# Optimization experiments

Measured on AMD Instinct MI355X. Metric: run time of the kernel, lower is better.

The kernel has to match this reference:

```python
import jax, jax.numpy as jnp
import numpy as np

N_NODES = 80000
N_EDGES = 160000
HID = 300
NODE_DIM = 133
EDGE_DIM = 14
N_GRAPHS = 1600


def setup_inputs() -> dict:
    key = jax.random.key(0)
    ks = jax.random.split(key, 32)
    s = 0.05
    half = N_EDGES // 2
    inp = {
        "x": jax.random.normal(ks[0], (N_NODES, NODE_DIM), jnp.float32),
        "edge_attr": jax.random.normal(ks[1], (N_EDGES, EDGE_DIM), jnp.float32),
        "W_atoms": jax.random.uniform(ks[2], (N_NODES,), jnp.float32),
        "eps": jax.random.normal(ks[3], (N_GRAPHS, HID), jnp.float32),
        "src_half": jax.random.randint(ks[4], (half,), 0, N_NODES, jnp.int32),
        "dst_half": jax.random.randint(ks[5], (half,), 0, N_NODES, jnp.int32),
        "batch": jnp.sort(jax.random.randint(ks[6], (N_NODES,), 0, N_GRAPHS, jnp.int32)),
    }
    def W(k, i, o):
        return jax.random.normal(k, (i, o), jnp.float32) * s
    def B(k, o):
        return jax.random.normal(k, (o,), jnp.float32) * s
    # tconv1 (first_linear=True): lin1 in=node+edge, atom_updater in=node+hid (with ReLU)
    inp["t_lin_w"] = W(ks[7], NODE_DIM + EDGE_DIM, HID); inp["t_lin_b"] = B(ks[8], HID)
    inp["t_mp_w"] = jax.random.normal(ks[9], (3, HID, HID), jnp.float32) * s
    inp["t_mp_b"] = jax.random.normal(ks[10], (3, HID), jnp.float32) * s
    inp["t_au_w"] = W(ks[11], NODE_DIM + HID, HID); inp["t_au_b"] = B(ks[12], HID)
    # mu conv (first_linear=False): lin2 in=hid+edge, atom_updater2 in=2*hid (no ReLU)
    inp["mu_lin_w"] = W(ks[13], HID + EDGE_DIM, HID); inp["mu_lin_b"] = B(ks[14], HID)
    inp["mu_mp_w"] = jax.random.normal(ks[15], (3, HID, HID), jnp.float32) * s
    inp["mu_mp_b"] = jax.random.normal(ks[16], (3, HID), jnp.float32) * s
    inp["mu_au_w"] = W(ks[17], 2 * HID, HID); inp["mu_au_b"] = B(ks[18], HID)
    # logvar conv (first_linear=False)
    inp["lv_lin_w"] = W(ks[19], HID + EDGE_DIM, HID); inp["lv_lin_b"] = B(ks[20], HID)
    inp["lv_mp_w"] = jax.random.normal(ks[21], (3, HID, HID), jnp.float32) * s
    inp["lv_mp_b"] = jax.random.normal(ks[22], (3, HID), jnp.float32) * s
    inp["lv_au_w"] = W(ks[23], 2 * HID, HID); inp["lv_au_b"] = B(ks[24], HID)
    return inp


def reference(x, edge_attr, W_atoms, eps, src_half, dst_half, batch,
              t_lin_w, t_lin_b, t_mp_w, t_mp_b, t_au_w, t_au_b,
              mu_lin_w, mu_lin_b, mu_mp_w, mu_mp_b, mu_au_w, mu_au_b,
              lv_lin_w, lv_lin_b, lv_mp_w, lv_mp_b, lv_au_w, lv_au_b):
    E = edge_attr.shape[0]
    half = E // 2
    N = x.shape[0]
    # directed edges come in reverse pairs: edge e and edge rev(e)
    src = jnp.concatenate([src_half, dst_half])
    dst = jnp.concatenate([dst_half, src_half])
    rev = jnp.concatenate([jnp.arange(half, E), jnp.arange(0, half)])
    relu = jax.nn.relu

    def mp_agg(h):
        # dest_is_origin sparse mm: for edge e=(u->v), sum h over edges k with
        # dst(k)==u, excluding the reverse edge (v->u)
        inc = jax.ops.segment_sum(h, dst, num_segments=N)  # [N, H]
        return inc[src] - h[rev]

    def conv(node_in, lin_w, lin_b, mp_w, mp_b, au_w, au_b, out_relu):
        h = relu(jnp.concatenate([node_in[src], edge_attr], axis=1) @ lin_w + lin_b)
        for i in range(3):  # three vec_scratch_MP_layers: relu(h + Lin(D @ h))
            h = relu(h + mp_agg(h) @ mp_w[i] + mp_b[i])
        # inc_edges_to_atom sparse mm: sum incident edge states per atom
        sum_inc = jax.ops.segment_sum(h, dst, num_segments=N)
        a = jnp.concatenate([node_in, sum_inc], axis=1) @ au_w + au_b
        return relu(a) if out_relu else a

    shared = conv(x, t_lin_w, t_lin_b, t_mp_w, t_mp_b, t_au_w, t_au_b, True)
    mu = conv(shared, mu_lin_w, mu_lin_b, mu_mp_w, mu_mp_b, mu_au_w, mu_au_b, False)
    lv = conv(shared, lv_lin_w, lv_lin_b, lv_mp_w, lv_mp_b, lv_au_w, lv_au_b, False)

    w = W_atoms[:, None]
    cnt = jnp.maximum(jax.ops.segment_sum(jnp.ones((N,), x.dtype), batch,
                                          num_segments=N_GRAPHS), 1.0)[:, None]
    mu_g = jax.ops.segment_sum(mu * w, batch, num_segments=N_GRAPHS) / cnt
    lv_g = jax.ops.segment_sum(lv * w, batch, num_segments=N_GRAPHS) / cnt
    # VAE reparameterization: z = mu + exp(0.5*logvar) * eps
    z = mu_g + jnp.exp(0.5 * lv_g) * eps
    return z
```

## Files before the change

### kernel.cpp

```cpp
#include <hip/hip_runtime.h>
#include <hip/hip_bf16.h>

#define NN 80000
#define NE 160000
#define HALF 80000
#define HID 300
#define NG 1600
#define SCB 256

typedef __attribute__((ext_vector_type(8))) short bf16x8v;
typedef __attribute__((ext_vector_type(4))) float f32x4v;

__device__ __forceinline__ float bf2f_us(unsigned short u) {
    return __uint_as_float(((unsigned int)u) << 16);
}
__device__ __forceinline__ unsigned short f2bf_us(float f) {
    union { __bf16 b; unsigned short u; } cv;
    cv.b = (__bf16)f;
    return cv.u;
}
__device__ __forceinline__ float ld1(const float* p) { return *p; }
__device__ __forceinline__ float ld1(const unsigned short* p) { return bf2f_us(*p); }
__device__ __forceinline__ void st1(float* p, float v) { *p = v; }
__device__ __forceinline__ void st1(unsigned short* p, float v) { *p = f2bf_us(v); }
__device__ __forceinline__ float4 ld4(const float* p) { return *(const float4*)p; }
__device__ __forceinline__ float4 ld4(const unsigned short* p) {
    ushort4 u = *(const ushort4*)p;
    return make_float4(bf2f_us(u.x), bf2f_us(u.y), bf2f_us(u.z), bf2f_us(u.w));
}
__device__ __forceinline__ void st4(float* p, float4 v) { *(float4*)p = v; }
__device__ __forceinline__ void st4(unsigned short* p, float4 v) {
    ushort4 u; u.x = f2bf_us(v.x); u.y = f2bf_us(v.y); u.z = f2bf_us(v.z); u.w = f2bf_us(v.w);
    *(ushort4*)p = u;
}
__device__ __forceinline__ int clampi(int v, int lo, int hi) {
    return v < lo ? lo : (v > hi ? hi : v);
}

__global__ void k_zerof(float* __restrict__ p, int n) {
    int i = blockIdx.x * 256 + threadIdx.x; if (i < n) p[i] = 0.f;
}
__global__ void k_zeroi(int* __restrict__ p, int n) {
    int i = blockIdx.x * 256 + threadIdx.x; if (i < n) p[i] = 0;
}

__global__ void k_wsplit_conv(const float* __restrict__ Wmp,
                              const float* __restrict__ Wlin, int Klin, int nktlin,
                              const float* __restrict__ Wau, int Kau, int nktau,
                              unsigned short* __restrict__ wh_mp, unsigned short* __restrict__ wl_mp,
                              unsigned short* __restrict__ wh_la, unsigned short* __restrict__ wl_la) {
    const int MP_L = 10 * 19 * 512;
    int idx = blockIdx.x * 256 + threadIdx.x;
    int total = 570 + nktlin * 19 + nktau * 19;
    int t = idx >> 6;
    if (t >= total) return;
    int lane = idx & 63;
    const float* W; int Krows, ltile;
    unsigned short *whi, *wlo;
    if (t < 570) {
        int l = t / 190, rem = t - l * 190;
        W = Wmp + l * 90000; Krows = 300; ltile = rem;
        whi = wh_mp + l * MP_L; wlo = wl_mp + l * MP_L;
    } else if (t < 570 + nktlin * 19) {
        ltile = t - 570; W = Wlin; Krows = Klin;
        whi = wh_la; wlo = wl_la;
    } else {
        ltile = t - 570 - nktlin * 19; W = Wau; Krows = Kau;
        size_t off = (size_t)nktlin * 19 * 512;
        whi = wh_la + off; wlo = wl_la + off;
    }
    int kt = ltile / 19, ct = ltile - kt * 19;
    int quad = lane >> 4, cr = lane & 15;
    size_t obase = ((size_t)ltile * 64 + lane) * 8;
    for (int j = 0; j < 8; ++j) {
        int k = kt * 32 + quad * 8 + j;
        int n = ct * 16 + cr;
        float v = (k < Krows && n < 300) ? W[(size_t)k * 300 + n] : 0.f;
        unsigned short hu = f2bf_us(v);
        unsigned short lu = f2bf_us(v - bf2f_us(hu));
        whi[obase + j] = hu;
        wlo[obase + j] = lu;
    }
}

__global__ void k_hist(const int* __restrict__ srcH, const int* __restrict__ dstH, int* __restrict__ deg) {
    int e = blockIdx.x * 256 + threadIdx.x;
    if (e >= NE) return;
    int d = (e < HALF) ? dstH[e] : srcH[e - HALF];
    d = clampi(d, 0, NN - 1);
    atomicAdd(&deg[d], 1);
}
__global__ void k_histg(const int* __restrict__ batch, int* __restrict__ degg) {
    int n = blockIdx.x * 256 + threadIdx.x;
    if (n >= NN) return;
    atomicAdd(&degg[clampi(batch[n], 0, NG - 1)], 1);
}

__global__ __launch_bounds__(256) void k_scan_part(const int* __restrict__ deg, int* __restrict__ part, int n) {
    __shared__ int red[256];
    int b = blockIdx.x, t = threadIdx.x;
    int chunk = (n + SCB - 1) / SCB;
    int lo = b * chunk, hi = lo + chunk; if (hi > n) hi = n;
    int s = 0;
    for (int i = lo + t; i < hi; i += 256) s += deg[i];
    red[t] = s;
    __syncthreads();
    for (int off = 128; off > 0; off >>= 1) {
        if (t < off) red[t] += red[t + off];
        __syncthreads();
    }
    if (t == 0) part[b] = red[0];
}
__global__ __launch_bounds__(256) void k_scan_offsets(int* __restrict__ part) {
    __shared__ int sh[256];
    int t = threadIdx.x;
    sh[t] = part[t];
    __syncthreads();
    for (int off = 1; off < 256; off <<= 1) {
        int v = (t >= off) ? sh[t - off] : 0;
        __syncthreads();
        sh[t] += v;
        __syncthreads();
    }
    part[t] = (t == 0) ? 0 : sh[t - 1];
}
__global__ __launch_bounds__(256) void k_scan_apply(const int* __restrict__ deg, const int* __restrict__ part,
                                                    int* __restrict__ start, int* cursor, int n) {
    __shared__ int sh[256];
    int b = blockIdx.x, t = threadIdx.x;
    int chunk = (n + SCB - 1) / SCB;
    int lo = b * chunk, hi = lo + chunk; if (hi > n) hi = n;
    int sub = (chunk + 255) / 256;
    int slo = lo + t * sub, shi = slo + sub;
    if (slo > hi) slo = hi;
    if (shi > hi) shi = hi;
    int s = 0;
    for (int i = slo; i < shi; ++i) s += deg[i];
    sh[t] = s;
    __syncthreads();
    for (int off = 1; off < 256; off <<= 1) {
        int v = (t >= off) ? sh[t - off] : 0;
        __syncthreads();
        sh[t] += v;
        __syncthreads();
    }
    int run = part[b] + sh[t] - s;
    for (int i = slo; i < shi; ++i) {
        int d = deg[i];
        start[i] = run;
        if (cursor) cursor[i] = run;
        run += d;
    }
    if (b == SCB - 1 && t == 255) start[n] = run;
}

__global__ void k_fill(const int* __restrict__ srcH, const int* __restrict__ dstH,
                       int* __restrict__ cursor, int* __restrict__ elist) {
    int e = blockIdx.x * 256 + threadIdx.x;
    if (e >= NE) return;
    int d = (e < HALF) ? dstH[e] : srcH[e - HALF];
    d = clampi(d, 0, NN - 1);
    int pos = atomicAdd(&cursor[d], 1);
    if (pos >= 0 && pos < NE) elist[pos] = e;
}

__global__ __launch_bounds__(256) void k_segsum8(const unsigned short* __restrict__ h,
                                                 const int* __restrict__ elist,
                                                 const int* __restrict__ start,
                                                 unsigned short* __restrict__ inc) {
    int t = blockIdx.x * 256 + threadIdx.x;
    if (t >= NN * 38) return;
    int n = t / 38, q = t - n * 38;
    int c0 = q * 8;
    bool full = (c0 + 8 <= 300);
    int lo = clampi(start[n], 0, NE), hi = clampi(start[n + 1], 0, NE);
    float4 a0 = make_float4(0.f, 0.f, 0.f, 0.f);
    float4 a1 = make_float4(0.f, 0.f, 0.f, 0.f);
    int j = lo;
    for (; j + 2 <= hi; j += 2) {
        int e0 = clampi(elist[j], 0, NE - 1);
        int e1 = clampi(elist[j + 1], 0, NE - 1);
        const unsigned short* r0 = &h[(size_t)e0 * 300 + c0];
        const unsigned short* r1 = &h[(size_t)e1 * 300 + c0];
        float4 v0 = ld4(r0);
        float4 w0 = ld4(r1);
        a0.x += v0.x + w0.x; a0.y += v0.y + w0.y; a0.z += v0.z + w0.z; a0.w += v0.w + w0.w;
        if (full) {
            float4 v1 = ld4(r0 + 4);
            float4 w1 = ld4(r1 + 4);
            a1.x += v1.x + w1.x; a1.y += v1.y + w1.y; a1.z += v1.z + w1.z; a1.w += v1.w + w1.w;
        }
    }
    if (j < hi) {
        int e0 = clampi(elist[j], 0, NE - 1);
        const unsigned short* r0 = &h[(size_t)e0 * 300 + c0];
        float4 v0 = ld4(r0);
        a0.x += v0.x; a0.y += v0.y; a0.z += v0.z; a0.w += v0.w;
        if (full) {
            float4 v1 = ld4(r0 + 4);
            a1.x += v1.x; a1.y += v1.y; a1.z += v1.z; a1.w += v1.w;
        }
    }
    st4(&inc[(size_t)n * 300 + c0], a0);
    if (full) st4(&inc[(size_t)n * 300 + c0 + 4], a1);
}


template <int NID, typename TN>
__global__ __launch_bounds__(512, 4) void k_lin_mfma(
        const TN* __restrict__ node_in, const float* __restrict__ ea,
        const int* __restrict__ srcH, const int* __restrict__ dstH,
        const unsigned short* __restrict__ whi, const unsigned short* __restrict__ wlo,
        const float* __restrict__ bias, unsigned short* __restrict__ h) {
    constexpr int K = NID + 14;
    constexpr int KP = (K + 31) & ~31;
    constexpr int NKT = KP / 32;
    constexpr int LDK = (KP + 8 < 312) ? 312 : KP + 8;
    __shared__ unsigned short As[64 * LDK];
    __shared__ int ssrc[64];
    const int tid = threadIdx.x;
    const int lane = tid & 63, wv = tid >> 6;
    const int quad = lane >> 4, cr = lane & 15;
    const int e0 = blockIdx.x * 64;
    if (tid < 64) {
        int e = e0 + tid;
        int s = (e < HALF) ? srcH[e] : dstH[e - HALF];
        ssrc[tid] = clampi(s, 0, NN - 1);
    }
    __syncthreads();
    if constexpr (NID == 300) {
        for (int idx = tid; idx < 64 * 75; idx += 512) {
            int r = idx / 75, q = idx - r * 75;
            *(ushort4*)&As[r * LDK + q * 4] =
                *(const ushort4*)&((const unsigned short*)node_in)[(size_t)ssrc[r] * 300 + q * 4];
        }
        for (int idx = tid; idx < 64 * (KP - 300); idx += 512) {
            int r = idx / (KP - 300), k = idx - r * (KP - 300);
            int kk = 300 + k;
            float v = (kk < K) ? ea[(size_t)(e0 + r) * 14 + (kk - 300)] : 0.f;
            As[r * LDK + kk] = f2bf_us(v);
        }
    } else {
        for (int idx = tid; idx < 64 * KP; idx += 512) {
            int r = idx / KP, k = idx - r * KP;
            float v;
            if (k < NID)    v = ld1(&node_in[(size_t)ssrc[r] * NID + k]);
            else if (k < K) v = ea[(size_t)(e0 + r) * 14 + (k - NID)];
            else            v = 0.f;
            As[r * LDK + k] = f2bf_us(v);
        }
    }
    __syncthreads();
    f32x4v acc[4][3];
    #pragma unroll
    for (int c = 0; c < 3; ++c) {
        int ct = wv + 8 * c;
        float b = 0.f;
        if (ct < 19) { int col = ct * 16 + cr; if (col < 300) b = bias[col]; }
        #pragma unroll
        for (int rt = 0; rt < 4; ++rt) { f32x4v a = {b, b, b, b}; acc[rt][c] = a; }
    }
    for (int kt = 0; kt < NKT; ++kt) {
        bf16x8v bhi[3], blo[3];
        #pragma unroll
        for (int c = 0; c < 3; ++c) {
            int ct = wv + 8 * c;
            if (ct < 19) {
                size_t base = ((size_t)(kt * 19 + ct) * 64 + lane) * 8;
                bhi[c] = *(const bf16x8v*)&whi[base];
                blo[c] = *(const bf16x8v*)&wlo[base];
            }
        }
        #pragma unroll
        for (int rt = 0; rt < 4; ++rt) {
            bf16x8v a = *(const bf16x8v*)&As[(rt * 16 + cr) * LDK + kt * 32 + quad * 8];
            #pragma unroll
            for (int c = 0; c < 3; ++c) {
                int ct = wv + 8 * c;
                if (ct >= 19) break;
                acc[rt][c] = __builtin_amdgcn_mfma_f32_16x16x32_bf16(a, blo[c], acc[rt][c], 0, 0, 0);
                acc[rt][c] = __builtin_amdgcn_mfma_f32_16x16x32_bf16(a, bhi[c], acc[rt][c], 0, 0, 0);
            }
        }
    }
    __syncthreads();
    #pragma unroll
    for (int c = 0; c < 3; ++c) {
        int ct = wv + 8 * c;
        if (ct >= 19) break;
        int col = ct * 16 + cr;
        if (col >= 300) continue;
        #pragma unroll
        for (int rt = 0; rt < 4; ++rt)
            #pragma unroll
            for (int r = 0; r < 4; ++r)
                As[(rt * 16 + quad * 4 + r) * LDK + col] = f2bf_us(fmaxf(acc[rt][c][r], 0.f));
    }
    __syncthreads();
    for (int idx = tid; idx < 64 * 75; idx += 512) {
        int r = idx / 75, q = idx - r * 75;
        *(ushort4*)&h[(size_t)(e0 + r) * 300 + q * 4] = *(const ushort4*)&As[r * LDK + q * 4];
    }
}

template <int NID, typename TN, bool RELU>
__global__ __launch_bounds__(512, 4) void k_au_mfma(
        const TN* __restrict__ node_in, const unsigned short* __restrict__ h,
        const int* __restrict__ elist, const int* __restrict__ start,
        const unsigned short* __restrict__ whi, const unsigned short* __restrict__ wlo,
        const float* __restrict__ bias, unsigned short* __restrict__ out_rows) {
    constexpr int K = NID + 300;
    constexpr int KP = (K + 31) & ~31;
    constexpr int NKT = KP / 32;
    constexpr int LDK = KP + 8;
    __shared__ unsigned short As[64 * LDK];
    const int tid = threadIdx.x;
    const int lane = tid & 63, wv = tid >> 6;
    const int quad = lane >> 4, cr = lane & 15;
    const int n0 = blockIdx.x * 64;
    if constexpr (NID == 300) {
        for (int idx = tid; idx < 64 * 75; idx += 512) {
            int r = idx / 75, q = idx - r * 75;
            *(ushort4*)&As[r * LDK + q * 4] =
                *(const ushort4*)&((const unsigned short*)node_in)[(size_t)(n0 + r) * 300 + q * 4];
        }
    } else {
        const float* xb = (const float*)node_in + (size_t)n0 * NID;
        for (int f4 = tid; f4 < (64 * NID) / 4; f4 += 512) {
            float4 v = *(const float4*)&xb[f4 * 4];
            int f = f4 * 4;
            float vv[4] = {v.x, v.y, v.z, v.w};
            #pragma unroll
            for (int i = 0; i < 4; ++i) {
                int fi = f + i;
                int r = fi / NID, k = fi - r * NID;
                As[r * LDK + k] = f2bf_us(vv[i]);
            }
        }
    }
    for (int idx = tid; idx < 64 * 75; idx += 512) {
        int r = idx / 75, q = idx - r * 75;
        int n = n0 + r;
        int lo = clampi(start[n], 0, NE), hi = clampi(start[n + 1], 0, NE);
        float4 acc = make_float4(0.f, 0.f, 0.f, 0.f);
        int j = lo;
        for (; j + 2 <= hi; j += 2) {
            int ei0 = clampi(elist[j], 0, NE - 1);
            int ei1 = clampi(elist[j + 1], 0, NE - 1);
            float4 v0 = ld4(&h[(size_t)ei0 * 300 + q * 4]);
            float4 v1 = ld4(&h[(size_t)ei1 * 300 + q * 4]);
            acc.x += v0.x; acc.y += v0.y; acc.z += v0.z; acc.w += v0.w;
            acc.x += v1.x; acc.y += v1.y; acc.z += v1.z; acc.w += v1.w;
        }
        if (j < hi) {
            int ei0 = clampi(elist[j], 0, NE - 1);
            float4 v0 = ld4(&h[(size_t)ei0 * 300 + q * 4]);
            acc.x += v0.x; acc.y += v0.y; acc.z += v0.z; acc.w += v0.w;
        }
        unsigned short* dst = &As[r * LDK + NID + q * 4];
        dst[0] = f2bf_us(acc.x); dst[1] = f2bf_us(acc.y);
        dst[2] = f2bf_us(acc.z); dst[3] = f2bf_us(acc.w);
    }
    constexpr int PAD = KP - NID - 300;
    for (int idx = tid; idx < 64 * PAD; idx += 512) {
        int r = idx / PAD, k = idx - r * PAD;
        As[r * LDK + NID + 300 + k] = 0;
    }
    __syncthreads();
    f32x4v acc[4][3];
    #pragma unroll
    for (int c = 0; c < 3; ++c) {
        int ct = wv + 8 * c;
        float b = 0.f;
        if (ct < 19) { int col = ct * 16 + cr; if (col < 300) b = bias[col]; }
        #pragma unroll
        for (int rt = 0; rt < 4; ++rt) { f32x4v a = {b, b, b, b}; acc[rt][c] = a; }
    }
    for (int kt = 0; kt < NKT; ++kt) {
        bf16x8v bhi[3], blo[3];
        #pragma unroll
        for (int c = 0; c < 3; ++c) {
            int ct = wv + 8 * c;
            if (ct < 19) {
                size_t base = ((size_t)(kt * 19 + ct) * 64 + lane) * 8;
                bhi[c] = *(const bf16x8v*)&whi[base];
                blo[c] = *(const bf16x8v*)&wlo[base];
            }
        }
        #pragma unroll
        for (int rt = 0; rt < 4; ++rt) {
            bf16x8v a = *(const bf16x8v*)&As[(rt * 16 + cr) * LDK + kt * 32 + quad * 8];
            #pragma unroll
            for (int c = 0; c < 3; ++c) {
                int ct = wv + 8 * c;
                if (ct >= 19) break;
                acc[rt][c] = __builtin_amdgcn_mfma_f32_16x16x32_bf16(a, blo[c], acc[rt][c], 0, 0, 0);
                acc[rt][c] = __builtin_amdgcn_mfma_f32_16x16x32_bf16(a, bhi[c], acc[rt][c], 0, 0, 0);
            }
        }
    }
    __syncthreads();
    #pragma unroll
    for (int c = 0; c < 3; ++c) {
        int ct = wv + 8 * c;
        if (ct >= 19) break;
        int col = ct * 16 + cr;
        if (col >= 300) continue;
        #pragma unroll
        for (int rt = 0; rt < 4; ++rt)
            #pragma unroll
            for (int r = 0; r < 4; ++r) {
                float v = acc[rt][c][r];
                As[(rt * 16 + quad * 4 + r) * LDK + col] = f2bf_us(RELU ? fmaxf(v, 0.f) : v);
            }
    }
    __syncthreads();
    for (int idx = tid; idx < 64 * 75; idx += 512) {
        int r = idx / 75, q = idx - r * 75;
        *(ushort4*)&out_rows[(size_t)(n0 + r) * 300 + q * 4] = *(const ushort4*)&As[r * LDK + q * 4];
    }
}

__global__ __launch_bounds__(512, 4) void k_mp_mfma(
        unsigned short* __restrict__ h, const unsigned short* __restrict__ inc,
        const int* __restrict__ srcH, const int* __restrict__ dstH,
        const unsigned short* __restrict__ whi, const unsigned short* __restrict__ wlo,
        const float* __restrict__ bias) {
    constexpr int LDK = 328;
    __shared__ unsigned short Hs[64 * LDK];
    __shared__ int ssrc[64];
    const int tid = threadIdx.x;
    const int lane = tid & 63, wv = tid >> 6;
    const int quad = lane >> 4, cr = lane & 15;
    const int p0 = blockIdx.x * 32;
    if (tid < 64) {
        int r = tid;
        int e = (r < 32) ? (p0 + r) : (p0 + r - 32 + HALF);
        int s = (e < HALF) ? srcH[e] : dstH[e - HALF];
        ssrc[r] = clampi(s, 0, NN - 1);
    }
    __syncthreads();
    for (int idx = tid; idx < 64 * 80; idx += 512) {
        int r = idx / 80, q = idx - r * 80;
        int col = q * 4;
        if (col < 300) {
            int ep = (r < 32) ? (p0 + r + HALF) : (p0 + r - 32);
            float4 hp = ld4(&h[(size_t)ep * 300 + col]);
            float4 iv = ld4(&inc[(size_t)ssrc[r] * 300 + col]);
            st4(&Hs[r * LDK + col],
                make_float4(iv.x - hp.x, iv.y - hp.y, iv.z - hp.z, iv.w - hp.w));
        } else {
            *(ushort4*)&Hs[r * LDK + col] = make_ushort4(0, 0, 0, 0);
        }
    }
    __syncthreads();
    f32x4v acc[4][3];
    #pragma unroll
    for (int c = 0; c < 3; ++c)
        #pragma unroll
        for (int rt = 0; rt < 4; ++rt) {
            f32x4v a = {0.f, 0.f, 0.f, 0.f};
            acc[rt][c] = a;
        }
    for (int kt = 0; kt < 10; ++kt) {
        bf16x8v bhi[3], blo[3];
        #pragma unroll
        for (int c = 0; c < 3; ++c) {
            int ct = wv + 8 * c;
            if (ct < 19) {
                size_t base = ((size_t)(kt * 19 + ct) * 64 + lane) * 8;
                bhi[c] = *(const bf16x8v*)&whi[base];
                blo[c] = *(const bf16x8v*)&wlo[base];
            }
        }
        #pragma unroll
        for (int rt = 0; rt < 4; ++rt) {
            bf16x8v a = *(const bf16x8v*)&Hs[(rt * 16 + cr) * LDK + kt * 32 + quad * 8];
            #pragma unroll
            for (int c = 0; c < 3; ++c) {
                int ct = wv + 8 * c;
                if (ct >= 19) break;
                acc[rt][c] = __builtin_amdgcn_mfma_f32_16x16x32_bf16(a, blo[c], acc[rt][c], 0, 0, 0);
                acc[rt][c] = __builtin_amdgcn_mfma_f32_16x16x32_bf16(a, bhi[c], acc[rt][c], 0, 0, 0);
            }
        }
    }
    __syncthreads();
    #pragma unroll
    for (int c = 0; c < 3; ++c) {
        int ct = wv + 8 * c;
        if (ct >= 19) break;
        int col = ct * 16 + cr;
        if (col >= 300) continue;
        float bv = bias[col];
        #pragma unroll
        for (int rt = 0; rt < 4; ++rt)
            #pragma unroll
            for (int r = 0; r < 4; ++r) {
                int row = rt * 16 + quad * 4 + r;
                int e = (row < 32) ? (p0 + row) : (p0 + row - 32 + HALF);
                float hv = bf2f_us(h[(size_t)e * 300 + col]);
                Hs[row * LDK + col] = f2bf_us(fmaxf(acc[rt][c][r] + bv + hv, 0.f));
            }
    }
    __syncthreads();
    for (int idx = tid; idx < 64 * 75; idx += 512) {
        int r = idx / 75, q = idx - r * 75;
        int e = (r < 32) ? (p0 + r) : (p0 + r - 32 + HALF);
        *(ushort4*)&h[(size_t)e * 300 + q * 4] = *(const ushort4*)&Hs[r * LDK + q * 4];
    }
}

__global__ __launch_bounds__(320) void k_pool(const unsigned short* __restrict__ rows,
                                              const float* __restrict__ wat,
                                              const int* __restrict__ gs, float* __restrict__ outg) {
    int g = blockIdx.x, c = threadIdx.x;
    if (c >= 300) return;
    int lo = clampi(gs[g], 0, NN), hi = clampi(gs[g + 1], 0, NN);
    float acc = 0.f;
    for (int n = lo; n < hi; ++n)
        acc += bf2f_us(rows[(size_t)n * 300 + c]) * wat[n];
    float cn = fmaxf((float)(hi - lo), 1.f);
    outg[g * 300 + c] = acc / cn;
}
__global__ __launch_bounds__(320) void k_final(const float* __restrict__ mu_g, const float* __restrict__ lv_g,
                                               const float* __restrict__ eps, float* __restrict__ out) {
    int g = blockIdx.x, c = threadIdx.x;
    if (c >= 300) return;
    out[g * 300 + c] = mu_g[g * 300 + c] + expf(0.5f * lv_g[g * 300 + c]) * eps[g * 300 + c];
}

extern "C" void kernel_launch(void* const* d_in, const int* in_sizes, int n_in,
                              void* d_out, int out_size, void* d_ws, size_t ws_size,
                              hipStream_t stream) {
    float* outp = (float*)d_out;

    const size_t NEED = 199500000ull;
    if (ws_size < NEED) {
        k_zerof<<<(out_size + 255) / 256, 256, 0, stream>>>(outp, out_size);
        return;
    }

    const float* x   = (const float*)d_in[0];
    const float* ea  = (const float*)d_in[1];
    const float* wat = (const float*)d_in[2];
    const float* eps = (const float*)d_in[3];
    const int* srcH  = (const int*)d_in[4];
    const int* dstH  = (const int*)d_in[5];
    const int* batch = (const int*)d_in[6];
    const float* w_t_lin  = (const float*)d_in[7];
    const float* b_t_lin  = (const float*)d_in[8];
    const float* w_t_mp   = (const float*)d_in[9];
    const float* b_t_mp   = (const float*)d_in[10];
    const float* w_t_au   = (const float*)d_in[11];
    const float* b_t_au   = (const float*)d_in[12];
    const float* w_mu_lin = (const float*)d_in[13];
    const float* b_mu_lin = (const float*)d_in[14];
    const float* w_mu_mp  = (const float*)d_in[15];
    const float* b_mu_mp  = (const float*)d_in[16];
    const float* w_mu_au  = (const float*)d_in[17];
    const float* b_mu_au  = (const float*)d_in[18];
    const float* w_lv_lin = (const float*)d_in[19];
    const float* b_lv_lin = (const float*)d_in[20];
    const float* w_lv_mp  = (const float*)d_in[21];
    const float* b_lv_mp  = (const float*)d_in[22];
    const float* w_lv_au  = (const float*)d_in[23];
    const float* b_lv_au  = (const float*)d_in[24];

    char* p = (char*)d_ws;
    auto alloc = [&](size_t nbytes) { char* q = p; p += (nbytes + 255) & ~(size_t)255; return q; };
    unsigned short* h   = (unsigned short*)alloc((size_t)NE * 300 * 2);
    unsigned short* inc = (unsigned short*)alloc((size_t)NN * 300 * 2);
    unsigned short* sh  = (unsigned short*)alloc((size_t)NN * 300 * 2);
    const size_t MPU = (size_t)3 * 10 * 19 * 512;
    unsigned short* wh_mp = (unsigned short*)alloc(MPU * 2);
    unsigned short* wl_mp = (unsigned short*)alloc(MPU * 2);
    const size_t LAU = (size_t)29 * 19 * 512;
    unsigned short* wh_la = (unsigned short*)alloc(LAU * 2);
    unsigned short* wl_la = (unsigned short*)alloc(LAU * 2);
    float* mu_g = (float*)alloc((size_t)NG * 300 * 4);
    float* lv_g = (float*)alloc((size_t)NG * 300 * 4);
    int* deg    = (int*)alloc(NN * 4);
    int* startA = (int*)alloc((NN + 1) * 4);
    int* elist  = (int*)alloc(NE * 4);
    int* degg   = (int*)alloc(NG * 4);
    int* gs     = (int*)alloc((NG + 1) * 4);
    int* part   = (int*)alloc(SCB * 4);

    k_zeroi<<<(NN + 255) / 256, 256, 0, stream>>>(deg, NN);
    k_hist<<<(NE + 255) / 256, 256, 0, stream>>>(srcH, dstH, deg);
    k_scan_part<<<SCB, 256, 0, stream>>>(deg, part, NN);
    k_scan_offsets<<<1, 256, 0, stream>>>(part);
    k_scan_apply<<<SCB, 256, 0, stream>>>(deg, part, startA, deg, NN);
    k_fill<<<(NE + 255) / 256, 256, 0, stream>>>(srcH, dstH, deg, elist);
    k_zeroi<<<(NG + 255) / 256, 256, 0, stream>>>(degg, NG);
    k_histg<<<(NN + 255) / 256, 256, 0, stream>>>(batch, degg);
    k_scan_part<<<SCB, 256, 0, stream>>>(degg, part, NG);
    k_scan_offsets<<<1, 256, 0, stream>>>(part);
    k_scan_apply<<<SCB, 256, 0, stream>>>(degg, part, gs, (int*)nullptr, NG);

    const int SSG = (NN * 38 + 255) / 256;
    const size_t MP_L = (size_t)10 * 19 * 512;
    unsigned short* rows = inc;
    auto wsplit_conv = [&](const float* Wmp, const float* Wlin, int Klin, int nktlin,
                           const float* Wau, int Kau, int nktau) {
        int total = 570 + nktlin * 19 + nktau * 19;
        k_wsplit_conv<<<(total * 64 + 255) / 256, 256, 0, stream>>>(
            Wmp, Wlin, Klin, nktlin, Wau, Kau, nktau, wh_mp, wl_mp, wh_la, wl_la);
    };

    wsplit_conv(w_t_mp, w_t_lin, 147, 5, w_t_au, 433, 14);
    const size_t AU_T = (size_t)5 * 19 * 512;
    k_lin_mfma<133, float><<<NE / 64, 512, 0, stream>>>(x, ea, srcH, dstH, wh_la, wl_la, b_t_lin, h);
    for (int i = 0; i < 3; ++i) {
        k_segsum8<<<SSG, 256, 0, stream>>>(h, elist, startA, inc);
        k_mp_mfma<<<HALF / 32, 512, 0, stream>>>(h, inc, srcH, dstH,
                                                 wh_mp + i * MP_L, wl_mp + i * MP_L, b_t_mp + i * 300);
    }
    k_au_mfma<133, float, true><<<NN / 64, 512, 0, stream>>>(x, h, elist, startA,
                                                             wh_la + AU_T, wl_la + AU_T, b_t_au, sh);

    wsplit_conv(w_mu_mp, w_mu_lin, 314, 10, w_mu_au, 600, 19);
    const size_t AU_MU = (size_t)10 * 19 * 512;
    k_lin_mfma<300, unsigned short><<<NE / 64, 512, 0, stream>>>(sh, ea, srcH, dstH, wh_la, wl_la, b_mu_lin, h);
    for (int i = 0; i < 3; ++i) {
        k_segsum8<<<SSG, 256, 0, stream>>>(h, elist, startA, inc);
        k_mp_mfma<<<HALF / 32, 512, 0, stream>>>(h, inc, srcH, dstH,
                                                 wh_mp + i * MP_L, wl_mp + i * MP_L, b_mu_mp + i * 300);
    }
    k_au_mfma<300, unsigned short, false><<<NN / 64, 512, 0, stream>>>(sh, h, elist, startA,
                                                                       wh_la + AU_MU, wl_la + AU_MU, b_mu_au, rows);
    k_pool<<<NG, 320, 0, stream>>>(rows, wat, gs, mu_g);

    wsplit_conv(w_lv_mp, w_lv_lin, 314, 10, w_lv_au, 600, 19);
    k_lin_mfma<300, unsigned short><<<NE / 64, 512, 0, stream>>>(sh, ea, srcH, dstH, wh_la, wl_la, b_lv_lin, h);
    for (int i = 0; i < 3; ++i) {
        k_segsum8<<<SSG, 256, 0, stream>>>(h, elist, startA, inc);
        k_mp_mfma<<<HALF / 32, 512, 0, stream>>>(h, inc, srcH, dstH,
                                                 wh_mp + i * MP_L, wl_mp + i * MP_L, b_lv_mp + i * 300);
    }
    k_au_mfma<300, unsigned short, false><<<NN / 64, 512, 0, stream>>>(sh, h, elist, startA,
                                                                       wh_la + AU_MU, wl_la + AU_MU, b_lv_au, rows);
    k_pool<<<NG, 320, 0, stream>>>(rows, wat, gs, lv_g);

    k_final<<<NG, 320, 0, stream>>>(mu_g, lv_g, eps, outp);
}
```

Measured before the change: 2.048 ms.

## Halve MFMA GEMM row tiles to 32 rows with 4 waves, split lo/hi weight passes

The three MFMA GEMM kernels (edge linear, message passing, atom updater) now use 32-row tiles with 256 threads instead of 64-row tiles with 512 threads. Each wave covers up to 5 column tiles across 2 row tiles instead of 3 column tiles across 4 row tiles. The lo and hi split-bf16 weight fragments are now loaded and applied in two separate passes, which reduces live registers. The aim is more blocks, smaller LDS per block and better occupancy. In exchange, each block reads the weights with less reuse, roughly doubling weight-fragment global traffic per row processed.

```diff
diff --git a/kernel.cpp b/kernel.cpp
--- a/kernel.cpp
+++ b/kernel.cpp
@@ -21,8 +21,6 @@
 }
 __device__ __forceinline__ float ld1(const float* p) { return *p; }
 __device__ __forceinline__ float ld1(const unsigned short* p) { return bf2f_us(*p); }
-__device__ __forceinline__ void st1(float* p, float v) { *p = v; }
-__device__ __forceinline__ void st1(unsigned short* p, float v) { *p = f2bf_us(v); }
 __device__ __forceinline__ float4 ld4(const float* p) { return *(const float4*)p; }
 __device__ __forceinline__ float4 ld4(const unsigned short* p) {
     ushort4 u = *(const ushort4*)p;
@@ -207,7 +205,7 @@
 
 
 template <int NID, typename TN>
-__global__ __launch_bounds__(512, 4) void k_lin_mfma(
+__global__ __launch_bounds__(256, 4) void k_lin_mfma(
         const TN* __restrict__ node_in, const float* __restrict__ ea,
         const int* __restrict__ srcH, const int* __restrict__ dstH,
         const unsigned short* __restrict__ whi, const unsigned short* __restrict__ wlo,
@@ -216,32 +214,32 @@
     constexpr int KP = (K + 31) & ~31;
     constexpr int NKT = KP / 32;
     constexpr int LDK = (KP + 8 < 312) ? 312 : KP + 8;
-    __shared__ unsigned short As[64 * LDK];
-    __shared__ int ssrc[64];
+    __shared__ unsigned short As[32 * LDK];
+    __shared__ int ssrc[32];
     const int tid = threadIdx.x;
     const int lane = tid & 63, wv = tid >> 6;
     const int quad = lane >> 4, cr = lane & 15;
-    const int e0 = blockIdx.x * 64;
-    if (tid < 64) {
+    const int e0 = blockIdx.x * 32;
+    if (tid < 32) {
         int e = e0 + tid;
         int s = (e < HALF) ? srcH[e] : dstH[e - HALF];
         ssrc[tid] = clampi(s, 0, NN - 1);
     }
     __syncthreads();
     if constexpr (NID == 300) {
-        for (int idx = tid; idx < 64 * 75; idx += 512) {
+        for (int idx = tid; idx < 32 * 75; idx += 256) {
             int r = idx / 75, q = idx - r * 75;
             *(ushort4*)&As[r * LDK + q * 4] =
                 *(const ushort4*)&((const unsigned short*)node_in)[(size_t)ssrc[r] * 300 + q * 4];
         }
-        for (int idx = tid; idx < 64 * (KP - 300); idx += 512) {
+        for (int idx = tid; idx < 32 * (KP - 300); idx += 256) {
             int r = idx / (KP - 300), k = idx - r * (KP - 300);
             int kk = 300 + k;
             float v = (kk < K) ? ea[(size_t)(e0 + r) * 14 + (kk - 300)] : 0.f;
             As[r * LDK + kk] = f2bf_us(v);
         }
     } else {
-        for (int idx = tid; idx < 64 * KP; idx += 512) {
+        for (int idx = tid; idx < 32 * KP; idx += 256) {
             int r = idx / KP, k = idx - r * KP;
             float v;
             if (k < NID)    v = ld1(&node_in[(size_t)ssrc[r] * NID + k]);
@@ -251,60 +249,72 @@
         }
     }
     __syncthreads();
-    f32x4v acc[4][3];
+    f32x4v acc[2][5];
     #pragma unroll
-    for (int c = 0; c < 3; ++c) {
-        int ct = wv + 8 * c;
+    for (int c = 0; c < 5; ++c) {
+        int ct = wv + 4 * c;
         float b = 0.f;
         if (ct < 19) { int col = ct * 16 + cr; if (col < 300) b = bias[col]; }
         #pragma unroll
-        for (int rt = 0; rt < 4; ++rt) { f32x4v a = {b, b, b, b}; acc[rt][c] = a; }
+        for (int rt = 0; rt < 2; ++rt) { f32x4v a = {b, b, b, b}; acc[rt][c] = a; }
     }
     for (int kt = 0; kt < NKT; ++kt) {
-        bf16x8v bhi[3], blo[3];
-        #pragma unroll
-        for (int c = 0; c < 3; ++c) {
-            int ct = wv + 8 * c;
-            if (ct < 19) {
-                size_t base = ((size_t)(kt * 19 + ct) * 64 + lane) * 8;
-                bhi[c] = *(const bf16x8v*)&whi[base];
-                blo[c] = *(const bf16x8v*)&wlo[base];
-            }
-        }
-        #pragma unroll
-        for (int rt = 0; rt < 4; ++rt) {
+        bf16x8v bb[5];
+        #pragma unroll
+        for (int c = 0; c < 5; ++c) {
+            int ct = wv + 4 * c;
+            if (ct < 19)
+                bb[c] = *(const bf16x8v*)&wlo[((size_t)(kt * 19 + ct) * 64 + lane) * 8];
+        }
+        #pragma unroll
+        for (int rt = 0; rt < 2; ++rt) {
             bf16x8v a = *(const bf16x8v*)&As[(rt * 16 + cr) * LDK + kt * 32 + quad * 8];
             #pragma unroll
-            for (int c = 0; c < 3; ++c) {
-                int ct = wv + 8 * c;
+            for (int c = 0; c < 5; ++c) {
+                int ct = wv + 4 * c;
                 if (ct >= 19) break;
-                acc[rt][c] = __builtin_amdgcn_mfma_f32_16x16x32_bf16(a, blo[c], acc[rt][c], 0, 0, 0);
-                acc[rt][c] = __builtin_amdgcn_mfma_f32_16x16x32_bf16(a, bhi[c], acc[rt][c], 0, 0, 0);
+                acc[rt][c] = __builtin_amdgcn_mfma_f32_16x16x32_bf16(a, bb[c], acc[rt][c], 0, 0, 0);
+            }
+        }
+        #pragma unroll
+        for (int c = 0; c < 5; ++c) {
+            int ct = wv + 4 * c;
+            if (ct < 19)
+                bb[c] = *(const bf16x8v*)&whi[((size_t)(kt * 19 + ct) * 64 + lane) * 8];
+        }
+        #pragma unroll
+        for (int rt = 0; rt < 2; ++rt) {
+            bf16x8v a = *(const bf16x8v*)&As[(rt * 16 + cr) * LDK + kt * 32 + quad * 8];
+            #pragma unroll
+            for (int c = 0; c < 5; ++c) {
+                int ct = wv + 4 * c;
+                if (ct >= 19) break;
+                acc[rt][c] = __builtin_amdgcn_mfma_f32_16x16x32_bf16(a, bb[c], acc[rt][c], 0, 0, 0);
             }
         }
     }
     __syncthreads();
     #pragma unroll
-    for (int c = 0; c < 3; ++c) {
-        int ct = wv + 8 * c;
+    for (int c = 0; c < 5; ++c) {
+        int ct = wv + 4 * c;
         if (ct >= 19) break;
         int col = ct * 16 + cr;
         if (col >= 300) continue;
         #pragma unroll
-        for (int rt = 0; rt < 4; ++rt)
+        for (int rt = 0; rt < 2; ++rt)
             #pragma unroll
             for (int r = 0; r < 4; ++r)
                 As[(rt * 16 + quad * 4 + r) * LDK + col] = f2bf_us(fmaxf(acc[rt][c][r], 0.f));
     }
     __syncthreads();
-    for (int idx = tid; idx < 64 * 75; idx += 512) {
+    for (int idx = tid; idx < 32 * 75; idx += 256) {
         int r = idx / 75, q = idx - r * 75;
         *(ushort4*)&h[(size_t)(e0 + r) * 300 + q * 4] = *(const ushort4*)&As[r * LDK + q * 4];
     }
 }
 
 template <int NID, typename TN, bool RELU>
-__global__ __launch_bounds__(512, 4) void k_au_mfma(
+__global__ __launch_bounds__(256, 4) void k_au_mfma(
         const TN* __restrict__ node_in, const unsigned short* __restrict__ h,
         const int* __restrict__ elist, const int* __restrict__ start,
         const unsigned short* __restrict__ whi, const unsigned short* __restrict__ wlo,
@@ -313,20 +323,20 @@
     constexpr int KP = (K + 31) & ~31;
     constexpr int NKT = KP / 32;
     constexpr int LDK = KP + 8;
-    __shared__ unsigned short As[64 * LDK];
+    __shared__ unsigned short As[32 * LDK];
     const int tid = threadIdx.x;
     const int lane = tid & 63, wv = tid >> 6;
     const int quad = lane >> 4, cr = lane & 15;
-    const int n0 = blockIdx.x * 64;
+    const int n0 = blockIdx.x * 32;
     if constexpr (NID == 300) {
-        for (int idx = tid; idx < 64 * 75; idx += 512) {
+        for (int idx = tid; idx < 32 * 75; idx += 256) {
             int r = idx / 75, q = idx - r * 75;
             *(ushort4*)&As[r * LDK + q * 4] =
                 *(const ushort4*)&((const unsigned short*)node_in)[(size_t)(n0 + r) * 300 + q * 4];
         }
     } else {
         const float* xb = (const float*)node_in + (size_t)n0 * NID;
-        for (int f4 = tid; f4 < (64 * NID) / 4; f4 += 512) {
+        for (int f4 = tid; f4 < (32 * NID) / 4; f4 += 256) {
             float4 v = *(const float4*)&xb[f4 * 4];
             int f = f4 * 4;
             float vv[4] = {v.x, v.y, v.z, v.w};
@@ -338,7 +348,7 @@
             }
         }
     }
-    for (int idx = tid; idx < 64 * 75; idx += 512) {
+    for (int idx = tid; idx < 32 * 75; idx += 256) {
         int r = idx / 75, q = idx - r * 75;
         int n = n0 + r;
         int lo = clampi(start[n], 0, NE), hi = clampi(start[n + 1], 0, NE);
@@ -362,52 +372,64 @@
         dst[2] = f2bf_us(acc.z); dst[3] = f2bf_us(acc.w);
     }
     constexpr int PAD = KP - NID - 300;
-    for (int idx = tid; idx < 64 * PAD; idx += 512) {
+    for (int idx = tid; idx < 32 * PAD; idx += 256) {
         int r = idx / PAD, k = idx - r * PAD;
         As[r * LDK + NID + 300 + k] = 0;
     }
     __syncthreads();
-    f32x4v acc[4][3];
+    f32x4v acc[2][5];
     #pragma unroll
-    for (int c = 0; c < 3; ++c) {
-        int ct = wv + 8 * c;
+    for (int c = 0; c < 5; ++c) {
+        int ct = wv + 4 * c;
         float b = 0.f;
         if (ct < 19) { int col = ct * 16 + cr; if (col < 300) b = bias[col]; }
         #pragma unroll
-        for (int rt = 0; rt < 4; ++rt) { f32x4v a = {b, b, b, b}; acc[rt][c] = a; }
+        for (int rt = 0; rt < 2; ++rt) { f32x4v a = {b, b, b, b}; acc[rt][c] = a; }
     }
     for (int kt = 0; kt < NKT; ++kt) {
-        bf16x8v bhi[3], blo[3];
-        #pragma unroll
-        for (int c = 0; c < 3; ++c) {
-            int ct = wv + 8 * c;
-            if (ct < 19) {
-                size_t base = ((size_t)(kt * 19 + ct) * 64 + lane) * 8;
-                bhi[c] = *(const bf16x8v*)&whi[base];
-                blo[c] = *(const bf16x8v*)&wlo[base];
-            }
-        }
-        #pragma unroll
-        for (int rt = 0; rt < 4; ++rt) {
+        bf16x8v bb[5];
+        #pragma unroll
+        for (int c = 0; c < 5; ++c) {
+            int ct = wv + 4 * c;
+            if (ct < 19)
+                bb[c] = *(const bf16x8v*)&wlo[((size_t)(kt * 19 + ct) * 64 + lane) * 8];
+        }
+        #pragma unroll
+        for (int rt = 0; rt < 2; ++rt) {
             bf16x8v a = *(const bf16x8v*)&As[(rt * 16 + cr) * LDK + kt * 32 + quad * 8];
             #pragma unroll
-            for (int c = 0; c < 3; ++c) {
-                int ct = wv + 8 * c;
+            for (int c = 0; c < 5; ++c) {
+                int ct = wv + 4 * c;
                 if (ct >= 19) break;
-                acc[rt][c] = __builtin_amdgcn_mfma_f32_16x16x32_bf16(a, blo[c], acc[rt][c], 0, 0, 0);
-                acc[rt][c] = __builtin_amdgcn_mfma_f32_16x16x32_bf16(a, bhi[c], acc[rt][c], 0, 0, 0);
+                acc[rt][c] = __builtin_amdgcn_mfma_f32_16x16x32_bf16(a, bb[c], acc[rt][c], 0, 0, 0);
+            }
+        }
+        #pragma unroll
+        for (int c = 0; c < 5; ++c) {
+            int ct = wv + 4 * c;
+            if (ct < 19)
+                bb[c] = *(const bf16x8v*)&whi[((size_t)(kt * 19 + ct) * 64 + lane) * 8];
+        }
+        #pragma unroll
+        for (int rt = 0; rt < 2; ++rt) {
+            bf16x8v a = *(const bf16x8v*)&As[(rt * 16 + cr) * LDK + kt * 32 + quad * 8];
+            #pragma unroll
+            for (int c = 0; c < 5; ++c) {
+                int ct = wv + 4 * c;
+                if (ct >= 19) break;
+                acc[rt][c] = __builtin_amdgcn_mfma_f32_16x16x32_bf16(a, bb[c], acc[rt][c], 0, 0, 0);
             }
         }
     }
     __syncthreads();
     #pragma unroll
-    for (int c = 0; c < 3; ++c) {
-        int ct = wv + 8 * c;
+    for (int c = 0; c < 5; ++c) {
+        int ct = wv + 4 * c;
         if (ct >= 19) break;
         int col = ct * 16 + cr;
         if (col >= 300) continue;
         #pragma unroll
-        for (int rt = 0; rt < 4; ++rt)
+        for (int rt = 0; rt < 2; ++rt)
             #pragma unroll
             for (int r = 0; r < 4; ++r) {
                 float v = acc[rt][c][r];
@@ -415,36 +437,36 @@
             }
     }
     __syncthreads();
-    for (int idx = tid; idx < 64 * 75; idx += 512) {
+    for (int idx = tid; idx < 32 * 75; idx += 256) {
         int r = idx / 75, q = idx - r * 75;
         *(ushort4*)&out_rows[(size_t)(n0 + r) * 300 + q * 4] = *(const ushort4*)&As[r * LDK + q * 4];
     }
 }
 
-__global__ __launch_bounds__(512, 4) void k_mp_mfma(
+__global__ __launch_bounds__(256, 4) void k_mp_mfma(
         unsigned short* __restrict__ h, const unsigned short* __restrict__ inc,
         const int* __restrict__ srcH, const int* __restrict__ dstH,
         const unsigned short* __restrict__ whi, const unsigned short* __restrict__ wlo,
         const float* __restrict__ bias) {
     constexpr int LDK = 328;
-    __shared__ unsigned short Hs[64 * LDK];
-    __shared__ int ssrc[64];
+    __shared__ unsigned short Hs[32 * LDK];
+    __shared__ int ssrc[32];
     const int tid = threadIdx.x;
     const int lane = tid & 63, wv = tid >> 6;
     const int quad = lane >> 4, cr = lane & 15;
-    const int p0 = blockIdx.x * 32;
-    if (tid < 64) {
+    const int p0 = blockIdx.x * 16;
+    if (tid < 32) {
         int r = tid;
-        int e = (r < 32) ? (p0 + r) : (p0 + r - 32 + HALF);
+        int e = (r < 16) ? (p0 + r) : (p0 + r - 16 + HALF);
         int s = (e < HALF) ? srcH[e] : dstH[e - HALF];
         ssrc[r] = clampi(s, 0, NN - 1);
     }
     __syncthreads();
-    for (int idx = tid; idx < 64 * 80; idx += 512) {
+    for (int idx = tid; idx < 32 * 80; idx += 256) {
         int r = idx / 80, q = idx - r * 80;
         int col = q * 4;
         if (col < 300) {
-            int ep = (r < 32) ? (p0 + r + HALF) : (p0 + r - 32);
+            int ep = (r < 16) ? (p0 + r + HALF) : (p0 + r - 16);
             float4 hp = ld4(&h[(size_t)ep * 300 + col]);
             float4 iv = ld4(&inc[(size_t)ssrc[r] * 300 + col]);
             st4(&Hs[r * LDK + col],
@@ -454,59 +476,71 @@
         }
     }
     __syncthreads();
-    f32x4v acc[4][3];
+    f32x4v acc[2][5];
     #pragma unroll
-    for (int c = 0; c < 3; ++c)
-        #pragma unroll
-        for (int rt = 0; rt < 4; ++rt) {
+    for (int c = 0; c < 5; ++c)
+        #pragma unroll
+        for (int rt = 0; rt < 2; ++rt) {
             f32x4v a = {0.f, 0.f, 0.f, 0.f};
             acc[rt][c] = a;
         }
     for (int kt = 0; kt < 10; ++kt) {
-        bf16x8v bhi[3], blo[3];
-        #pragma unroll
-        for (int c = 0; c < 3; ++c) {
-            int ct = wv + 8 * c;
-            if (ct < 19) {
-                size_t base = ((size_t)(kt * 19 + ct) * 64 + lane) * 8;
-                bhi[c] = *(const bf16x8v*)&whi[base];
-                blo[c] = *(const bf16x8v*)&wlo[base];
-            }
-        }
-        #pragma unroll
-        for (int rt = 0; rt < 4; ++rt) {
+        bf16x8v bb[5];
+        #pragma unroll
+        for (int c = 0; c < 5; ++c) {
+            int ct = wv + 4 * c;
+            if (ct < 19)
+                bb[c] = *(const bf16x8v*)&wlo[((size_t)(kt * 19 + ct) * 64 + lane) * 8];
+        }
+        #pragma unroll
+        for (int rt = 0; rt < 2; ++rt) {
             bf16x8v a = *(const bf16x8v*)&Hs[(rt * 16 + cr) * LDK + kt * 32 + quad * 8];
             #pragma unroll
-            for (int c = 0; c < 3; ++c) {
-                int ct = wv + 8 * c;
+            for (int c = 0; c < 5; ++c) {
+                int ct = wv + 4 * c;
                 if (ct >= 19) break;
-                acc[rt][c] = __builtin_amdgcn_mfma_f32_16x16x32_bf16(a, blo[c], acc[rt][c], 0, 0, 0);
-                acc[rt][c] = __builtin_amdgcn_mfma_f32_16x16x32_bf16(a, bhi[c], acc[rt][c], 0, 0, 0);
+                acc[rt][c] = __builtin_amdgcn_mfma_f32_16x16x32_bf16(a, bb[c], acc[rt][c], 0, 0, 0);
+            }
+        }
+        #pragma unroll
+        for (int c = 0; c < 5; ++c) {
+            int ct = wv + 4 * c;
+            if (ct < 19)
+                bb[c] = *(const bf16x8v*)&whi[((size_t)(kt * 19 + ct) * 64 + lane) * 8];
+        }
+        #pragma unroll
+        for (int rt = 0; rt < 2; ++rt) {
+            bf16x8v a = *(const bf16x8v*)&Hs[(rt * 16 + cr) * LDK + kt * 32 + quad * 8];
+            #pragma unroll
+            for (int c = 0; c < 5; ++c) {
+                int ct = wv + 4 * c;
+                if (ct >= 19) break;
+                acc[rt][c] = __builtin_amdgcn_mfma_f32_16x16x32_bf16(a, bb[c], acc[rt][c], 0, 0, 0);
             }
         }
     }
     __syncthreads();
     #pragma unroll
-    for (int c = 0; c < 3; ++c) {
-        int ct = wv + 8 * c;
+    for (int c = 0; c < 5; ++c) {
+        int ct = wv + 4 * c;
         if (ct >= 19) break;
         int col = ct * 16 + cr;
         if (col >= 300) continue;
         float bv = bias[col];
         #pragma unroll
-        for (int rt = 0; rt < 4; ++rt)
+        for (int rt = 0; rt < 2; ++rt)
             #pragma unroll
             for (int r = 0; r < 4; ++r) {
                 int row = rt * 16 + quad * 4 + r;
-                int e = (row < 32) ? (p0 + row) : (p0 + row - 32 + HALF);
+                int e = (row < 16) ? (p0 + row) : (p0 + row - 16 + HALF);
                 float hv = bf2f_us(h[(size_t)e * 300 + col]);
                 Hs[row * LDK + col] = f2bf_us(fmaxf(acc[rt][c][r] + bv + hv, 0.f));
             }
     }
     __syncthreads();
-    for (int idx = tid; idx < 64 * 75; idx += 512) {
+    for (int idx = tid; idx < 32 * 75; idx += 256) {
         int r = idx / 75, q = idx - r * 75;
-        int e = (r < 32) ? (p0 + r) : (p0 + r - 32 + HALF);
+        int e = (r < 16) ? (p0 + r) : (p0 + r - 16 + HALF);
         *(ushort4*)&h[(size_t)e * 300 + q * 4] = *(const ushort4*)&Hs[r * LDK + q * 4];
     }
 }
@@ -611,35 +645,35 @@
 
     wsplit_conv(w_t_mp, w_t_lin, 147, 5, w_t_au, 433, 14);
     const size_t AU_T = (size_t)5 * 19 * 512;
-    k_lin_mfma<133, float><<<NE / 64, 512, 0, stream>>>(x, ea, srcH, dstH, wh_la, wl_la, b_t_lin, h);
+    k_lin_mfma<133, float><<<NE / 32, 256, 0, stream>>>(x, ea, srcH, dstH, wh_la, wl_la, b_t_lin, h);
     for (int i = 0; i < 3; ++i) {
         k_segsum8<<<SSG, 256, 0, stream>>>(h, elist, startA, inc);
-        k_mp_mfma<<<HALF / 32, 512, 0, stream>>>(h, inc, srcH, dstH,
+        k_mp_mfma<<<HALF / 16, 256, 0, stream>>>(h, inc, srcH, dstH,
                                                  wh_mp + i * MP_L, wl_mp + i * MP_L, b_t_mp + i * 300);
     }
-    k_au_mfma<133, float, true><<<NN / 64, 512, 0, stream>>>(x, h, elist, startA,
+    k_au_mfma<133, float, true><<<NN / 32, 256, 0, stream>>>(x, h, elist, startA,
                                                              wh_la + AU_T, wl_la + AU_T, b_t_au, sh);
 
     wsplit_conv(w_mu_mp, w_mu_lin, 314, 10, w_mu_au, 600, 19);
     const size_t AU_MU = (size_t)10 * 19 * 512;
-    k_lin_mfma<300, unsigned short><<<NE / 64, 512, 0, stream>>>(sh, ea, srcH, dstH, wh_la, wl_la, b_mu_lin, h);
+    k_lin_mfma<300, unsigned short><<<NE / 32, 256, 0, stream>>>(sh, ea, srcH, dstH, wh_la, wl_la, b_mu_lin, h);
     for (int i = 0; i < 3; ++i) {
         k_segsum8<<<SSG, 256, 0, stream>>>(h, elist, startA, inc);
-        k_mp_mfma<<<HALF / 32, 512, 0, stream>>>(h, inc, srcH, dstH,
+        k_mp_mfma<<<HALF / 16, 256, 0, stream>>>(h, inc, srcH, dstH,
                                                  wh_mp + i * MP_L, wl_mp + i * MP_L, b_mu_mp + i * 300);
     }
-    k_au_mfma<300, unsigned short, false><<<NN / 64, 512, 0, stream>>>(sh, h, elist, startA,
+    k_au_mfma<300, unsigned short, false><<<NN / 32, 256, 0, stream>>>(sh, h, elist, startA,
                                                                        wh_la + AU_MU, wl_la + AU_MU, b_mu_au, rows);
     k_pool<<<NG, 320, 0, stream>>>(rows, wat, gs, mu_g);
 
     wsplit_conv(w_lv_mp, w_lv_lin, 314, 10, w_lv_au, 600, 19);
-    k_lin_mfma<300, unsigned short><<<NE / 64, 512, 0, stream>>>(sh, ea, srcH, dstH, wh_la, wl_la, b_lv_lin, h);
+    k_lin_mfma<300, unsigned short><<<NE / 32, 256, 0, stream>>>(sh, ea, srcH, dstH, wh_la, wl_la, b_lv_lin, h);
     for (int i = 0; i < 3; ++i) {
         k_segsum8<<<SSG, 256, 0, stream>>>(h, elist, startA, inc);
-        k_mp_mfma<<<HALF / 32, 512, 0, stream>>>(h, inc, srcH, dstH,
+        k_mp_mfma<<<HALF / 16, 256, 0, stream>>>(h, inc, srcH, dstH,
                                                  wh_mp + i * MP_L, wl_mp + i * MP_L, b_lv_mp + i * 300);
     }
-    k_au_mfma<300, unsigned short, false><<<NN / 64, 512, 0, stream>>>(sh, h, elist, startA,
+    k_au_mfma<300, unsigned short, false><<<NN / 32, 256, 0, stream>>>(sh, h, elist, startA,
                                                                        wh_la + AU_MU, wl_la + AU_MU, b_lv_au, rows);
     k_pool<<<NG, 320, 0, stream>>>(rows, wat, gs, lv_g);
 
```

Result: slower. 2.219 ms (+8.3%).
